# Performance work log

Hardware: AMD Instinct MI355X
Metric: run time of the kernel (lower is better)

The kernel has to match this reference:

```python
import jax, jax.numpy as jnp
import numpy as np

B = 65536          # graphs (agents)
NODES_PER = 9      # 1 torso + 8 joints
N = B * NODES_PER
D = 64
SOFTPLUS_BIAS = float(np.log(np.expm1(1.0)))  # biased_softplus_1.0 from NormalParamExtractor


def _star_edges():
    # bidirectional torso<->joint star per 9-node graph
    base = np.arange(B, dtype=np.int64) * NODES_PER          # torso ids [B]
    torso = np.repeat(base, 8)                               # [8B]
    joint = (base[:, None] + np.arange(1, 9, dtype=np.int64)[None, :]).reshape(-1)  # [8B]
    src = np.concatenate([torso, joint])                     # torso->joint, joint->torso
    dst = np.concatenate([joint, torso])
    return jnp.asarray(np.stack([src, dst], axis=0))         # [2, 16B]


def setup_inputs() -> dict:
    key = jax.random.key(0)
    ks = jax.random.split(key, 12)
    s = lambda fan_in: 1.0 / np.sqrt(fan_in)
    inp = {
        "x": jax.random.normal(ks[0], (N, 11), dtype=jnp.float32),
        "edge_index": _star_edges(),
        # input projections
        "W_joint": jax.random.uniform(ks[1], (2, D), jnp.float32, -s(2), s(2)),
        "b_joint": jnp.zeros((D,), jnp.float32),
        "W_torso": jax.random.uniform(ks[2], (11, D), jnp.float32, -s(11), s(11)),
        "b_torso": jnp.zeros((D,), jnp.float32),
        # GraphConv 1: lin_rel (bias) on aggregated neighbors + lin_root (no bias)
        "W_rel1": jax.random.uniform(ks[3], (D, D), jnp.float32, -s(D), s(D)),
        "b_rel1": jnp.zeros((D,), jnp.float32),
        "W_root1": jax.random.uniform(ks[4], (D, D), jnp.float32, -s(D), s(D)),
        # GraphConv 2
        "W_rel2": jax.random.uniform(ks[5], (D, D), jnp.float32, -s(D), s(D)),
        "b_rel2": jnp.zeros((D,), jnp.float32),
        "W_root2": jax.random.uniform(ks[6], (D, D), jnp.float32, -s(D), s(D)),
        # 8 per-joint heads Linear(64, 2)
        "W_heads": jax.random.uniform(ks[7], (8, D, 2), jnp.float32, -s(D), s(D)),
        "b_heads": jnp.zeros((8, 2), jnp.float32),
    }
    return inp


def _graph_conv(h, src, dst, W_rel, b_rel, W_root, n):
    # GraphConv (aggr='add'): out[i] = lin_rel(sum_{j->i} h[j]) + lin_root(h[i])
    agg = jax.ops.segment_sum(h[src], dst, num_segments=n)   # [N, D]
    return agg @ W_rel + b_rel + h @ W_root


def reference(x, edge_index, W_joint, b_joint, W_torso, b_torso,
              W_rel1, b_rel1, W_root1, W_rel2, b_rel2, W_root2,
              W_heads, b_heads):
    n = x.shape[0]
    b = n // NODES_PER
    xg = x.reshape(b, NODES_PER, 11)
    h_torso = xg[:, :1, :] @ W_torso + b_torso              # [b, 1, D]  (node 0 of each graph)
    h_joint = xg[:, 1:, :2] @ W_joint + b_joint             # [b, 8, D]
    h = jnp.concatenate([h_torso, h_joint], axis=1).reshape(n, D)
    src, dst = edge_index[0], edge_index[1]
    h = jnp.tanh(_graph_conv(h, src, dst, W_rel1, b_rel1, W_root1, n))
    h = jnp.tanh(_graph_conv(h, src, dst, W_rel2, b_rel2, W_root2, n))
    joints = h.reshape(b, NODES_PER, D)[:, 1:, :]           # [b, 8, D]
    out = jnp.einsum('bjd,jdo->bjo', joints, W_heads) + b_heads  # [b, 8, 2]
    loc = out[..., 0]                                       # [b, 8]
    scale = jax.nn.softplus(out[..., 1] + SOFTPLUS_BIAS)    # biased_softplus_1.0
    return loc, scale
```

## Files before the change

kernel.cpp:

```cpp
#include <hip/hip_runtime.h>


typedef __attribute__((ext_vector_type(8))) short bf16x8;
typedef __attribute__((ext_vector_type(4))) float f32x4;

#define SOFTPLUS_BIAS 0.5413248546129181f
#define LDS_SB  24576
#define LDS_SZ  26624
#define FENCE() asm volatile("" ::: "memory")

__device__ __forceinline__ unsigned int cvtpk(float lo, float hi) {
  unsigned int r;
  asm("v_cvt_pk_bf16_f32 %0, %1, %2" : "=v"(r) : "v"(lo), "v"(hi));
  return r;
}
__device__ __forceinline__ float asf(unsigned int u) {
  union { unsigned int i; float f; } v; v.i = u; return v.f;
}
__device__ __forceinline__ unsigned short f2bf(float f) {
  union { float f; unsigned int i; } v; v.f = f;
  unsigned int lsb = (v.i >> 16) & 1u;
  return (unsigned short)((v.i + 0x7fffu + lsb) >> 16);
}
__device__ __forceinline__ float fast_tanh(float x) {
  float e = __expf(2.0f * x);
  return 1.0f - 2.0f * __builtin_amdgcn_rcpf(e + 1.0f);
}

__global__ void pack_weights(const float* __restrict__ Wrel1, const float* __restrict__ Wroot1,
                             const float* __restrict__ Wrel2, const float* __restrict__ Wroot2,
                             const float* __restrict__ Wheads, unsigned short* __restrict__ ws) {
  int id = blockIdx.x * 256 + threadIdx.x;
  if (id < 16384) {
    const float* W = (id < 4096) ? Wrel1 : (id < 8192) ? Wroot1 : (id < 12288) ? Wrel2 : Wroot2;
    int m = id & 4095;
    int e = m & 7, lane = (m >> 3) & 63, nt = (m >> 9) & 3, ks = m >> 11;
    int k = ((lane >> 4) << 3) + e + (ks << 5);
    int col = (nt << 4) + (lane & 15);
    ws[id] = f2bf(W[k * 64 + col]);
  } else if (id < 17408) {
    int m = id - 16384;
    int e = m & 7, lane = (m >> 3) & 63, ks = m >> 9;
    int k = ((lane >> 4) << 3) + e + (ks << 5);
    int c = lane & 15, j = c >> 1, o = c & 1;
    ws[id] = f2bf(Wheads[(j * 64 + k) * 2 + o]);
  }
}

__launch_bounds__(256, 3)
__global__ void actor_main(const float* __restrict__ x,
                           const float* __restrict__ Wj_g, const float* __restrict__ bj_g,
                           const float* __restrict__ Wt_g, const float* __restrict__ bt_g,
                           const float* __restrict__ brel1_g, const float* __restrict__ brel2_g,
                           const float* __restrict__ bh_g,
                           const unsigned short* __restrict__ wsw,
                           float* __restrict__ out) {
  __shared__ __align__(16) unsigned char smem[LDS_SZ];
  const int t = threadIdx.x;
  const int lane = t & 63;
  const int w = t >> 6;
  const int gbase = blockIdx.x << 4;
  const int l15 = lane & 15;
  const int q = lane >> 4;
  const int ks16 = q << 4;
  const unsigned HB = (unsigned)(w * 6144);
  const unsigned SB = (unsigned)(LDS_SB + w * 512);

  const bf16x8* wsv = reinterpret_cast<const bf16x8*>(wsw);

  float Wtr[11];
#pragma unroll
  for (int k = 0; k < 11; k++) Wtr[k] = Wt_g[k * 64 + lane];
  const float btr = bt_g[lane];
  const float Wj0 = Wj_g[lane], Wj1 = Wj_g[64 + lane], bjr = bj_g[lane];
  float brelA[4], brelB[4];
#pragma unroll
  for (int nt = 0; nt < 4; nt++) {
    brelA[nt] = brel1_g[l15 + (nt << 4)];
    brelB[nt] = brel2_g[l15 + (nt << 4)];
  }

  unsigned aggA[3];
#pragma unroll
  for (int mt = 0; mt < 3; mt++) {
    int r = (mt << 4) + l15;
    int g = (r * 43) >> 9;
    int node = r - 12 * g;
    int trow = 12 * g;
    aggA[mt] = (node == 0)
        ? (SB + g * 128 + (unsigned)(ks16 ^ (g << 4)))
        : (HB + trow * 128 + (unsigned)(ks16 ^ ((trow & 7) << 4)));
  }
  const unsigned h0b = HB + l15 * 128 + (unsigned)(ks16 ^ ((l15 & 7) << 4));

  const int w_u = __builtin_amdgcn_readfirstlane(w);
#pragma unroll
  for (int it = 0; it < 4; it++) {
    const float* __restrict__ xr = x + (size_t)(gbase + (w_u << 2) + it) * 99;
    float acc1 = btr;
#pragma unroll
    for (int k = 0; k < 11; k++) acc1 += xr[k] * Wtr[k];
    int trow = 12 * it;
    *reinterpret_cast<unsigned short*>(smem + HB + trow * 128 + ((2 * lane) ^ ((trow & 7) << 4))) =
        (unsigned short)cvtpk(acc1, acc1);
    float sx0 = 0.f, sx1 = 0.f;
#pragma unroll
    for (int j = 0; j < 8; j++) {
      float x0 = xr[11 + 11 * j];
      float x1 = xr[12 + 11 * j];
      sx0 += x0; sx1 += x1;
      float accj = bjr + x0 * Wj0 + x1 * Wj1;
      int row = 12 * it + 1 + j;
      *reinterpret_cast<unsigned short*>(smem + HB + row * 128 + ((2 * lane) ^ ((row & 7) << 4))) =
          (unsigned short)cvtpk(accj, accj);
    }
    float s = 8.0f * bjr + sx0 * Wj0 + sx1 * Wj1;
    *reinterpret_cast<unsigned short*>(smem + SB + it * 128 + ((2 * lane) ^ (it << 4))) =
        (unsigned short)cvtpk(s, s);
  }
  FENCE();

  f32x4 acc[3][4];
#pragma unroll
  for (int layer = 0; layer < 2; layer++) {
    const int lb = layer ? 1024 : 0;

    if (layer == 1) {
      int gS = lane >> 4, dq = lane & 15;
      int rb = dq << 3;
      float s0 = 0.f, s1 = 0.f, s2 = 0.f, s3 = 0.f;
#pragma unroll
      for (int j = 0; j < 8; j++) {
        int row = 12 * gS + 1 + j;
        uint2 p = *reinterpret_cast<const uint2*>(smem + HB + row * 128 + (rb ^ ((row & 7) << 4)));
        s0 += asf(p.x << 16); s1 += asf(p.x & 0xffff0000u);
        s2 += asf(p.y << 16); s3 += asf(p.y & 0xffff0000u);
      }
      uint2 o; o.x = cvtpk(s0, s1); o.y = cvtpk(s2, s3);
      *reinterpret_cast<uint2*>(smem + SB + gS * 128 + (rb ^ (gS << 4))) = o;
      FENCE();
    }

    bf16x8 bf[4][2];
#pragma unroll
    for (int nt = 0; nt < 4; nt++) {
      bf[nt][0] = wsv[lb + nt * 64 + lane];
      bf[nt][1] = wsv[lb + 256 + nt * 64 + lane];
    }
#pragma unroll
    for (int mt = 0; mt < 3; mt++) {
      bf16x8 ag0 = *reinterpret_cast<const bf16x8*>(smem + aggA[mt]);
      bf16x8 ag1 = *reinterpret_cast<const bf16x8*>(smem + (aggA[mt] ^ 64u));
#pragma unroll
      for (int nt = 0; nt < 4; nt++) {
        float br = layer ? brelB[nt] : brelA[nt];
        f32x4 c = {br, br, br, br};
        c = __builtin_amdgcn_mfma_f32_16x16x32_bf16(ag0, bf[nt][0], c, 0, 0, 0);
        acc[mt][nt] = __builtin_amdgcn_mfma_f32_16x16x32_bf16(ag1, bf[nt][1], c, 0, 0, 0);
      }
    }
#pragma unroll
    for (int nt = 0; nt < 4; nt++) {
      bf[nt][0] = wsv[lb + 512 + nt * 64 + lane];
      bf[nt][1] = wsv[lb + 768 + nt * 64 + lane];
    }
#pragma unroll
    for (int mt = 0; mt < 3; mt++) {
      bf16x8 a0 = *reinterpret_cast<const bf16x8*>(smem + h0b + mt * 2048);
      bf16x8 a1 = *reinterpret_cast<const bf16x8*>(smem + ((h0b + mt * 2048) ^ 64u));
#pragma unroll
      for (int nt = 0; nt < 4; nt++) {
        f32x4 c = __builtin_amdgcn_mfma_f32_16x16x32_bf16(a0, bf[nt][0], acc[mt][nt], 0, 0, 0);
        acc[mt][nt] = __builtin_amdgcn_mfma_f32_16x16x32_bf16(a1, bf[nt][1], c, 0, 0, 0);
      }
    }
    FENCE();

#pragma unroll
    for (int mt = 0; mt < 3; mt++) {
#pragma unroll
      for (int nt = 0; nt < 4; nt++) {
        unsigned p0 = cvtpk(fast_tanh(acc[mt][nt][0]), fast_tanh(acc[mt][nt][1]));
        unsigned p1 = cvtpk(fast_tanh(acc[mt][nt][2]), fast_tanh(acc[mt][nt][3]));
        const unsigned colp = (unsigned)((nt << 5) + 2 * l15);
#pragma unroll
        for (int i = 0; i < 4; i++) {
          int rr = (mt << 4) + (q << 2) + i;
          unsigned addr = HB + rr * 128 + (colp ^ (((q << 2) + i & 7) << 4));
          unsigned short v = (i == 0) ? (unsigned short)p0 : (i == 1) ? (unsigned short)(p0 >> 16)
                           : (i == 2) ? (unsigned short)p1 : (unsigned short)(p1 >> 16);
          *reinterpret_cast<unsigned short*>(smem + addr) = v;
        }
      }
    }
    FENCE();
  }

  {
    bf16x8 hb0 = wsv[2048 + lane];
    bf16x8 hb1 = wsv[2048 + 64 + lane];
#pragma unroll
    for (int u = 0; u < 2; u++) {
      int jw = (u << 4) + l15;
      int arow = 12 * (jw >> 3) + 1 + (jw & 7);
      unsigned ha = HB + arow * 128 + (unsigned)(ks16 ^ ((arow & 7) << 4));
      bf16x8 a0 = *reinterpret_cast<const bf16x8*>(smem + ha);
      bf16x8 a1 = *reinterpret_cast<const bf16x8*>(smem + (ha ^ 64u));
      f32x4 z = {0.f, 0.f, 0.f, 0.f};
      z = __builtin_amdgcn_mfma_f32_16x16x32_bf16(a0, hb0, z, 0, 0, 0);
      z = __builtin_amdgcn_mfma_f32_16x16x32_bf16(a1, hb1, z, 0, 0, 0);
#pragma unroll
      for (int i = 0; i < 4; i++) {
        int r = (u << 4) + (q << 2) + i;
        int gg = r >> 3, j2 = r & 7;
        size_t G = (size_t)(gbase + (w << 2) + gg);
        if (l15 == 2 * j2) {
          out[G * 8 + j2] = z[i] + bh_g[2 * j2];
        } else if (l15 == 2 * j2 + 1) {
          float zz = z[i] + bh_g[2 * j2 + 1] + SOFTPLUS_BIAS;
          float sp = (zz > 20.0f) ? zz : __logf(1.0f + __expf(zz));
          out[524288 + G * 8 + j2] = sp;
        }
      }
    }
  }
}

extern "C" void kernel_launch(void* const* d_in, const int* in_sizes, int n_in,
                              void* d_out, int out_size, void* d_ws, size_t ws_size,
                              hipStream_t stream) {
  const float* x      = (const float*)d_in[0];
  const float* Wj     = (const float*)d_in[2];
  const float* bj     = (const float*)d_in[3];
  const float* Wt     = (const float*)d_in[4];
  const float* bt     = (const float*)d_in[5];
  const float* Wrel1  = (const float*)d_in[6];
  const float* brel1  = (const float*)d_in[7];
  const float* Wroot1 = (const float*)d_in[8];
  const float* Wrel2  = (const float*)d_in[9];
  const float* brel2  = (const float*)d_in[10];
  const float* Wroot2 = (const float*)d_in[11];
  const float* Wheads = (const float*)d_in[12];
  const float* bh     = (const float*)d_in[13];
  unsigned short* ws16 = (unsigned short*)d_ws;
  float* out = (float*)d_out;

  hipLaunchKernelGGL(pack_weights, dim3(68), dim3(256), 0, stream,
                     Wrel1, Wroot1, Wrel2, Wroot2, Wheads, ws16);
  hipLaunchKernelGGL(actor_main, dim3(4096), dim3(256), 0, stream,
                     x, Wj, bj, Wt, bt, brel1, brel2, bh, ws16, out);
}
```

Before: 72.27 us.

## Swap MFMA operands to compute transposed GEMM and shrink LDS for occupancy

Restructures each GraphConv layer so the weights are the A operand and node features the B operand, computing the output transposed. This lets each output column tile be finished, tanh'd and written back as packed 8-byte stores, instead of holding a full 3x4 accumulator array and doing scattered 2-byte stores. The torso aggregate sums now live in a spare row (row 9 of each 12-row group) of the per-wave H buffer, which drops the separate SB region and shrinks LDS. Launch bounds rise from 3 to 4 blocks per SM. Weight fragments are reloaded from global per m-tile, and gathering all of H before writing back relies on each wave owning its own rows.

```diff
diff --git a/kernel.cpp b/kernel.cpp
--- a/kernel.cpp
+++ b/kernel.cpp
@@ -5,8 +5,7 @@
 typedef __attribute__((ext_vector_type(4))) float f32x4;
 
 #define SOFTPLUS_BIAS 0.5413248546129181f
-#define LDS_SB  24576
-#define LDS_SZ  26624
+#define LDS_SZ  24576
 #define FENCE() asm volatile("" ::: "memory")
 
 __device__ __forceinline__ unsigned int cvtpk(float lo, float hi) {
@@ -47,7 +46,7 @@
   }
 }
 
-__launch_bounds__(256, 3)
+__launch_bounds__(256, 4)
 __global__ void actor_main(const float* __restrict__ x,
                            const float* __restrict__ Wj_g, const float* __restrict__ bj_g,
                            const float* __restrict__ Wt_g, const float* __restrict__ bt_g,
@@ -63,8 +62,8 @@
   const int l15 = lane & 15;
   const int q = lane >> 4;
   const int ks16 = q << 4;
+  const int qo = q << 3;
   const unsigned HB = (unsigned)(w * 6144);
-  const unsigned SB = (unsigned)(LDS_SB + w * 512);
 
   const bf16x8* wsv = reinterpret_cast<const bf16x8*>(wsw);
 
@@ -73,25 +72,19 @@
   for (int k = 0; k < 11; k++) Wtr[k] = Wt_g[k * 64 + lane];
   const float btr = bt_g[lane];
   const float Wj0 = Wj_g[lane], Wj1 = Wj_g[64 + lane], bjr = bj_g[lane];
-  float brelA[4], brelB[4];
-#pragma unroll
-  for (int nt = 0; nt < 4; nt++) {
-    brelA[nt] = brel1_g[l15 + (nt << 4)];
-    brelB[nt] = brel2_g[l15 + (nt << 4)];
-  }
-
-  unsigned aggA[3];
-#pragma unroll
-  for (int mt = 0; mt < 3; mt++) {
-    int r = (mt << 4) + l15;
-    int g = (r * 43) >> 9;
-    int node = r - 12 * g;
-    int trow = 12 * g;
-    aggA[mt] = (node == 0)
-        ? (SB + g * 128 + (unsigned)(ks16 ^ (g << 4)))
-        : (HB + trow * 128 + (unsigned)(ks16 ^ ((trow & 7) << 4)));
-  }
-  const unsigned h0b = HB + l15 * 128 + (unsigned)(ks16 ^ ((l15 & 7) << 4));
+
+  unsigned aggB[3], hBr[3], wbase[3], swz[3];
+#pragma unroll
+  for (int nt = 0; nt < 3; nt++) {
+    int n = (nt << 4) + l15;
+    int g = (n * 43) >> 9;
+    int s = n - 12 * g;
+    int arow = (s == 0) ? (12 * g + 9) : (12 * g);
+    aggB[nt] = HB + arow * 128 + (unsigned)(ks16 ^ ((arow & 7) << 4));
+    hBr[nt]  = HB + n * 128 + (unsigned)(ks16 ^ ((n & 7) << 4));
+    wbase[nt] = HB + n * 128;
+    swz[nt] = (unsigned)((n & 7) << 4);
+  }
 
   const int w_u = __builtin_amdgcn_readfirstlane(w);
 #pragma unroll
@@ -115,12 +108,12 @@
           (unsigned short)cvtpk(accj, accj);
     }
     float s = 8.0f * bjr + sx0 * Wj0 + sx1 * Wj1;
-    *reinterpret_cast<unsigned short*>(smem + SB + it * 128 + ((2 * lane) ^ (it << 4))) =
+    int srow = 12 * it + 9;
+    *reinterpret_cast<unsigned short*>(smem + HB + srow * 128 + ((2 * lane) ^ ((srow & 7) << 4))) =
         (unsigned short)cvtpk(s, s);
   }
   FENCE();
 
-  f32x4 acc[3][4];
 #pragma unroll
   for (int layer = 0; layer < 2; layer++) {
     const int lb = layer ? 1024 : 0;
@@ -136,61 +129,47 @@
         s0 += asf(p.x << 16); s1 += asf(p.x & 0xffff0000u);
         s2 += asf(p.y << 16); s3 += asf(p.y & 0xffff0000u);
       }
+      int srow = 12 * gS + 9;
       uint2 o; o.x = cvtpk(s0, s1); o.y = cvtpk(s2, s3);
-      *reinterpret_cast<uint2*>(smem + SB + gS * 128 + (rb ^ (gS << 4))) = o;
+      *reinterpret_cast<uint2*>(smem + HB + srow * 128 + (rb ^ ((srow & 7) << 4))) = o;
       FENCE();
     }
 
-    bf16x8 bf[4][2];
-#pragma unroll
-    for (int nt = 0; nt < 4; nt++) {
-      bf[nt][0] = wsv[lb + nt * 64 + lane];
-      bf[nt][1] = wsv[lb + 256 + nt * 64 + lane];
-    }
-#pragma unroll
-    for (int mt = 0; mt < 3; mt++) {
-      bf16x8 ag0 = *reinterpret_cast<const bf16x8*>(smem + aggA[mt]);
-      bf16x8 ag1 = *reinterpret_cast<const bf16x8*>(smem + (aggA[mt] ^ 64u));
-#pragma unroll
-      for (int nt = 0; nt < 4; nt++) {
-        float br = layer ? brelB[nt] : brelA[nt];
-        f32x4 c = {br, br, br, br};
-        c = __builtin_amdgcn_mfma_f32_16x16x32_bf16(ag0, bf[nt][0], c, 0, 0, 0);
-        acc[mt][nt] = __builtin_amdgcn_mfma_f32_16x16x32_bf16(ag1, bf[nt][1], c, 0, 0, 0);
-      }
-    }
-#pragma unroll
-    for (int nt = 0; nt < 4; nt++) {
-      bf[nt][0] = wsv[lb + 512 + nt * 64 + lane];
-      bf[nt][1] = wsv[lb + 768 + nt * 64 + lane];
-    }
-#pragma unroll
-    for (int mt = 0; mt < 3; mt++) {
-      bf16x8 a0 = *reinterpret_cast<const bf16x8*>(smem + h0b + mt * 2048);
-      bf16x8 a1 = *reinterpret_cast<const bf16x8*>(smem + ((h0b + mt * 2048) ^ 64u));
-#pragma unroll
-      for (int nt = 0; nt < 4; nt++) {
-        f32x4 c = __builtin_amdgcn_mfma_f32_16x16x32_bf16(a0, bf[nt][0], acc[mt][nt], 0, 0, 0);
-        acc[mt][nt] = __builtin_amdgcn_mfma_f32_16x16x32_bf16(a1, bf[nt][1], c, 0, 0, 0);
-      }
-    }
-    FENCE();
-
-#pragma unroll
-    for (int mt = 0; mt < 3; mt++) {
-#pragma unroll
-      for (int nt = 0; nt < 4; nt++) {
-        unsigned p0 = cvtpk(fast_tanh(acc[mt][nt][0]), fast_tanh(acc[mt][nt][1]));
-        unsigned p1 = cvtpk(fast_tanh(acc[mt][nt][2]), fast_tanh(acc[mt][nt][3]));
-        const unsigned colp = (unsigned)((nt << 5) + 2 * l15);
-#pragma unroll
-        for (int i = 0; i < 4; i++) {
-          int rr = (mt << 4) + (q << 2) + i;
-          unsigned addr = HB + rr * 128 + (colp ^ (((q << 2) + i & 7) << 4));
-          unsigned short v = (i == 0) ? (unsigned short)p0 : (i == 1) ? (unsigned short)(p0 >> 16)
-                           : (i == 2) ? (unsigned short)p1 : (unsigned short)(p1 >> 16);
-          *reinterpret_cast<unsigned short*>(smem + addr) = v;
-        }
+    bf16x8 gA[3][2], gH[3][2];
+#pragma unroll
+    for (int nt = 0; nt < 3; nt++) {
+      gA[nt][0] = *reinterpret_cast<const bf16x8*>(smem + aggB[nt]);
+      gA[nt][1] = *reinterpret_cast<const bf16x8*>(smem + (aggB[nt] ^ 64u));
+      gH[nt][0] = *reinterpret_cast<const bf16x8*>(smem + hBr[nt]);
+      gH[nt][1] = *reinterpret_cast<const bf16x8*>(smem + (hBr[nt] ^ 64u));
+    }
+    const float4* brp = reinterpret_cast<const float4*>(layer ? brel2_g : brel1_g);
+    float4 bv[4];
+#pragma unroll
+    for (int m = 0; m < 4; m++) bv[m] = brp[(m << 2) + q];
+
+#pragma unroll
+    for (int m = 0; m < 4; m++) {
+      bf16x8 ar0 = wsv[lb + (m << 6) + lane];
+      bf16x8 ar1 = wsv[lb + 256 + (m << 6) + lane];
+      bf16x8 ao0 = wsv[lb + 512 + (m << 6) + lane];
+      bf16x8 ao1 = wsv[lb + 768 + (m << 6) + lane];
+      f32x4 c[3];
+#pragma unroll
+      for (int nt = 0; nt < 3; nt++) {
+        f32x4 cc = {bv[m].x, bv[m].y, bv[m].z, bv[m].w};
+        cc = __builtin_amdgcn_mfma_f32_16x16x32_bf16(ar0, gA[nt][0], cc, 0, 0, 0);
+        cc = __builtin_amdgcn_mfma_f32_16x16x32_bf16(ar1, gA[nt][1], cc, 0, 0, 0);
+        cc = __builtin_amdgcn_mfma_f32_16x16x32_bf16(ao0, gH[nt][0], cc, 0, 0, 0);
+        c[nt] = __builtin_amdgcn_mfma_f32_16x16x32_bf16(ao1, gH[nt][1], cc, 0, 0, 0);
+      }
+#pragma unroll
+      for (int nt = 0; nt < 3; nt++) {
+        uint2 o;
+        o.x = cvtpk(fast_tanh(c[nt][0]), fast_tanh(c[nt][1]));
+        o.y = cvtpk(fast_tanh(c[nt][2]), fast_tanh(c[nt][3]));
+        unsigned off = (unsigned)(((m << 5) | qo)) ^ swz[nt];
+        *reinterpret_cast<uint2*>(smem + wbase[nt] + off) = o;
       }
     }
     FENCE();
```

Result: faster. 68.61 us (-5.1%).
